# Performance work log

Hardware: AMD Instinct MI355X
Metric: run time of the kernel (lower is better)

Reference implementation:

```python
import jax, jax.numpy as jnp
import numpy as np

N_NODES = 100000
D = 128        # hidden_channels
H = 64         # hidden_size
E = 8192       # num_hyperedges
K = 32         # nodes per hyperedge (fixed group size)


def setup_inputs() -> dict:
    key = jax.random.key(0)
    k1, k2, k3, k4, k5, k6 = jax.random.split(key, 6)
    X = jax.random.normal(k1, (N_NODES, D), dtype=jnp.float32)
    idx = jax.random.randint(k2, (E, K), 0, N_NODES, dtype=jnp.int64)
    # per-hyperedge MLP params (torch Linear: y = x @ W.T + b), scaled like
    # torch's default uniform fan-in init magnitude
    W1 = jax.random.normal(k3, (E, H, D), dtype=jnp.float32) / np.sqrt(D)
    b1 = jax.random.normal(k4, (E, H), dtype=jnp.float32) / np.sqrt(D)
    W2 = jax.random.normal(k5, (E, H), dtype=jnp.float32) / np.sqrt(H)
    b2 = jax.random.normal(k6, (E,), dtype=jnp.float32) / np.sqrt(H)
    return {"X": X, "idx": idx, "W1": W1, "b1": b1, "W2": W2, "b2": b2}


def reference(X, idx, W1, b1, W2, b2):
    # gather node features per hyperedge: [E, K, D]
    x_he = X[idx]
    # per-edge 2-layer MLP scorer (leaky_relu slope 0.01 = torch default)
    h = jax.nn.leaky_relu(jnp.einsum('ekd,ehd->ekh', x_he, W1) + b1[:, None, :])
    w = jnp.einsum('ekh,eh->ek', h, W2) + b2[:, None]          # [E, K]
    beta = jax.nn.softmax(w, axis=1)                           # softmax over group
    z = jnp.einsum('ek,ekd->ed', beta, x_he)                   # weighted sum reduce
    Z = jnp.tanh(jax.nn.leaky_relu(z))                         # [E, D]
    return Z, beta
```

## Files before the change

kernel.cpp:

```cpp
#include <hip/hip_runtime.h>

#define E_EDGES 8192
#define KN 32
#define DD 128
#define HH 64
#define XPAD 8
#define EPB 4
#define NBLK (E_EDGES / EPB)

typedef __attribute__((ext_vector_type(8))) __bf16 bf16x8;
typedef __attribute__((ext_vector_type(4))) __bf16 bf16x4;
typedef __attribute__((ext_vector_type(4))) float f32x4;

__device__ __forceinline__ void sync_lds() {
    asm volatile("s_waitcnt lgkmcnt(0)" ::: "memory");
    __builtin_amdgcn_s_barrier();
    __builtin_amdgcn_sched_barrier(0);
}

__global__ __launch_bounds__(256, 4)
void he_attn_kernel(const float* __restrict__ X,
                    const int* __restrict__ idx,
                    const float* __restrict__ W1,
                    const float* __restrict__ b1,
                    const float* __restrict__ W2,
                    const float* __restrict__ b2,
                    float* __restrict__ Zout,
                    float* __restrict__ Bout)
{
    const int tid  = threadIdx.x;
    const int lane = tid & 63;
    const int wv   = tid >> 6;
    const int cl   = lane & 15;
    const int kg   = lane >> 4;
    const int ebase = blockIdx.x * EPB;

    const int r0 = tid >> 5;
    const int c0 = (tid & 31) * 4;
    const int j  = wv * 16 + cl;

    __shared__ unsigned short xsb[KN][DD + XPAD];
    __shared__ float wpart[4][KN];
    __shared__ float beta_s[KN];

    float b1v[EPB], w2v[EPB], b2v[EPB];
    #pragma unroll
    for (int t = 0; t < EPB; ++t) {
        b1v[t] = b1[(size_t)(ebase + t) * HH + j];
        w2v[t] = W2[(size_t)(ebase + t) * HH + j];
        b2v[t] = b2[ebase + t];
    }
    int rowc[4];
    #pragma unroll
    for (int it = 0; it < 4; ++it) rowc[it] = idx[(size_t)ebase * KN + r0 + 8 * it];
    float4 xr[4];
    #pragma unroll
    for (int it = 0; it < 4; ++it)
        xr[it] = *reinterpret_cast<const float4*>(X + (size_t)rowc[it] * DD + c0);
    float4 wf[8];
    {
        const float* W1r = W1 + ((size_t)ebase * HH + j) * DD;
        #pragma unroll
        for (int q = 0; q < 8; ++q)
            wf[q] = *reinterpret_cast<const float4*>(W1r + (q >> 1) * 32 + kg * 8 + (q & 1) * 4);
    }
    int rown[4];
    #pragma unroll
    for (int it = 0; it < 4; ++it)
        rown[it] = idx[(size_t)(ebase + 1) * KN + r0 + 8 * it];

    #pragma unroll
    for (int t = 0; t < EPB; ++t) {
        const int e = ebase + t;

        bf16x8 bb[4];
        #pragma unroll
        for (int kc = 0; kc < 4; ++kc) {
            float4 a = wf[2 * kc], b = wf[2 * kc + 1];
            bf16x8 v;
            v[0] = (__bf16)a.x; v[1] = (__bf16)a.y; v[2] = (__bf16)a.z; v[3] = (__bf16)a.w;
            v[4] = (__bf16)b.x; v[5] = (__bf16)b.y; v[6] = (__bf16)b.z; v[7] = (__bf16)b.w;
            bb[kc] = v;
        }

        sync_lds();

        #pragma unroll
        for (int it = 0; it < 4; ++it) {
            bf16x4 bv;
            bv[0] = (__bf16)xr[it].x; bv[1] = (__bf16)xr[it].y;
            bv[2] = (__bf16)xr[it].z; bv[3] = (__bf16)xr[it].w;
            *reinterpret_cast<bf16x4*>(&xsb[r0 + 8 * it][c0]) = bv;
        }

        if (t + 1 < EPB) {
            #pragma unroll
            for (int it = 0; it < 4; ++it)
                xr[it] = *reinterpret_cast<const float4*>(X + (size_t)rown[it] * DD + c0);
            const float* W1r = W1 + ((size_t)(e + 1) * HH + j) * DD;
            #pragma unroll
            for (int q = 0; q < 8; ++q)
                wf[q] = *reinterpret_cast<const float4*>(W1r + (q >> 1) * 32 + kg * 8 + (q & 1) * 4);
        }
        if (t + 2 < EPB) {
            #pragma unroll
            for (int it = 0; it < 4; ++it)
                rown[it] = idx[(size_t)(e + 2) * KN + r0 + 8 * it];
        }

        sync_lds();

        f32x4 acc0 = {0.f, 0.f, 0.f, 0.f}, acc1 = {0.f, 0.f, 0.f, 0.f};
        #pragma unroll
        for (int kc = 0; kc < 4; ++kc) {
            const int ds = kc * 32 + kg * 8;
            bf16x8 a0 = *reinterpret_cast<const bf16x8*>(&xsb[cl][ds]);
            bf16x8 a1 = *reinterpret_cast<const bf16x8*>(&xsb[16 + cl][ds]);
            acc0 = __builtin_amdgcn_mfma_f32_16x16x32_bf16(a0, bb[kc], acc0, 0, 0, 0);
            acc1 = __builtin_amdgcn_mfma_f32_16x16x32_bf16(a1, bb[kc], acc1, 0, 0, 0);
        }

        float pk[8];
        #pragma unroll
        for (int r = 0; r < 4; ++r) {
            float h0 = acc0[r] + b1v[t]; h0 = (h0 > 0.f) ? h0 : 0.01f * h0;
            float h1 = acc1[r] + b1v[t]; h1 = (h1 > 0.f) ? h1 : 0.01f * h1;
            pk[r]     = h0 * w2v[t];
            pk[4 + r] = h1 * w2v[t];
        }
        #pragma unroll
        for (int m = 1; m < 16; m <<= 1) {
            #pragma unroll
            for (int q = 0; q < 8; ++q) pk[q] += __shfl_xor(pk[q], m);
        }
        if (cl == 0) {
            #pragma unroll
            for (int r = 0; r < 4; ++r) {
                wpart[wv][kg * 4 + r]      = pk[r];
                wpart[wv][16 + kg * 4 + r] = pk[4 + r];
            }
        }

        sync_lds();

        if (tid < KN) {
            float v = b2v[t] + wpart[0][tid] + wpart[1][tid] + wpart[2][tid] + wpart[3][tid];
            float mx = v;
            #pragma unroll
            for (int off = 16; off >= 1; off >>= 1) mx = fmaxf(mx, __shfl_xor(mx, off));
            float ex = __expf(v - mx);
            float s = ex;
            #pragma unroll
            for (int off = 16; off >= 1; off >>= 1) s += __shfl_xor(s, off);
            float beta = ex / s;
            beta_s[tid] = beta;
            Bout[(size_t)e * KN + tid] = beta;
        }

        sync_lds();

        if (tid < DD) {
            float z = 0.f;
            #pragma unroll
            for (int k = 0; k < KN; ++k) {
                unsigned int bq = xsb[k][tid];
                z += beta_s[k] * __builtin_bit_cast(float, bq << 16);
            }
            z = (z > 0.f) ? z : 0.01f * z;
            Zout[(size_t)e * DD + tid] = tanhf(z);
        }
    }
}

extern "C" void kernel_launch(void* const* d_in, const int* in_sizes, int n_in,
                              void* d_out, int out_size, void* d_ws, size_t ws_size,
                              hipStream_t stream) {
    const float* X   = (const float*)d_in[0];
    const int*   idx = (const int*)d_in[1];
    const float* W1  = (const float*)d_in[2];
    const float* b1  = (const float*)d_in[3];
    const float* W2  = (const float*)d_in[4];
    const float* b2  = (const float*)d_in[5];
    float* Zout = (float*)d_out;
    float* Bout = Zout + (size_t)E_EDGES * DD;
    (void)in_sizes; (void)n_in; (void)out_size; (void)d_ws; (void)ws_size;
    he_attn_kernel<<<dim3(NBLK), dim3(256), 0, stream>>>(X, idx, W1, b1, W2, b2, Zout, Bout);
}
```

Baseline: 67.14 us.

## Assign one hyperedge per wavefront and replace block barriers with wave sync

Each wavefront now processes a whole hyperedge independently, doing its own gather, all four 16-wide H tiles of the MFMA scorer, softmax and weighted sum. This replaces the old layout where the four waves of a block split the H dimension of one edge and stepped through four edges in sequence. Block-wide barriers become wave-level syncs and the cross-wave partial-score reduction disappears. The cost is four times the LDS per block, less software prefetch across edges, and more serial MFMA work per wave.

```diff
diff --git a/kernel.cpp b/kernel.cpp
--- a/kernel.cpp
+++ b/kernel.cpp
@@ -4,18 +4,19 @@
 #define KN 32
 #define DD 128
 #define HH 64
-#define XPAD 8
-#define EPB 4
-#define NBLK (E_EDGES / EPB)
+#define XSTR (DD + 8)
 
 typedef __attribute__((ext_vector_type(8))) __bf16 bf16x8;
 typedef __attribute__((ext_vector_type(4))) __bf16 bf16x4;
 typedef __attribute__((ext_vector_type(4))) float f32x4;
 
-__device__ __forceinline__ void sync_lds() {
+__device__ __forceinline__ float bf2f(unsigned int u) {
+    return __builtin_bit_cast(float, u << 16);
+}
+
+__device__ __forceinline__ void wave_sync_lds() {
     asm volatile("s_waitcnt lgkmcnt(0)" ::: "memory");
-    __builtin_amdgcn_s_barrier();
-    __builtin_amdgcn_sched_barrier(0);
+    __builtin_amdgcn_wave_barrier();
 }
 
 __global__ __launch_bounds__(256, 4)
@@ -31,48 +32,59 @@
     const int tid  = threadIdx.x;
     const int lane = tid & 63;
     const int wv   = tid >> 6;
+    const int e    = blockIdx.x * 4 + wv;
     const int cl   = lane & 15;
     const int kg   = lane >> 4;
-    const int ebase = blockIdx.x * EPB;
 
-    const int r0 = tid >> 5;
-    const int c0 = (tid & 31) * 4;
-    const int j  = wv * 16 + cl;
+    __shared__ __align__(16) unsigned short xsb[4][KN][XSTR];
+    __shared__ __align__(16) float ws[4][KN];
 
-    __shared__ unsigned short xsb[KN][DD + XPAD];
-    __shared__ float wpart[4][KN];
-    __shared__ float beta_s[KN];
+    const int iv = idx[(size_t)e * KN + (lane & 31)];
+    float b1v[4], w2v[4];
+    #pragma unroll
+    for (int jt = 0; jt < 4; ++jt) {
+        b1v[jt] = b1[(size_t)e * HH + jt * 16 + cl];
+        w2v[jt] = W2[(size_t)e * HH + jt * 16 + cl];
+    }
+    const float b2v = b2[e];
 
-    float b1v[EPB], w2v[EPB], b2v[EPB];
+    const float* W1e = W1 + (size_t)e * HH * DD;
+    float4 wf[8];
     #pragma unroll
-    for (int t = 0; t < EPB; ++t) {
-        b1v[t] = b1[(size_t)(ebase + t) * HH + j];
-        w2v[t] = W2[(size_t)(ebase + t) * HH + j];
-        b2v[t] = b2[ebase + t];
+    for (int q = 0; q < 8; ++q)
+        wf[q] = *reinterpret_cast<const float4*>(
+            W1e + (size_t)cl * DD + (q >> 1) * 32 + kg * 8 + (q & 1) * 4);
+
+    const int rb = lane >> 5;
+    const int cc = lane & 31;
+    #pragma unroll
+    for (int hb = 0; hb < 2; ++hb) {
+        float4 xr[8];
+        #pragma unroll
+        for (int q = 0; q < 8; ++q) {
+            int row = __shfl(iv, rb + 2 * (hb * 8 + q));
+            xr[q] = reinterpret_cast<const float4*>(X)[(size_t)row * (DD / 4) + cc];
+        }
+        #pragma unroll
+        for (int q = 0; q < 8; ++q) {
+            bf16x4 bv;
+            bv[0] = (__bf16)xr[q].x; bv[1] = (__bf16)xr[q].y;
+            bv[2] = (__bf16)xr[q].z; bv[3] = (__bf16)xr[q].w;
+            *reinterpret_cast<bf16x4*>(&xsb[wv][rb + 2 * (hb * 8 + q)][cc * 4]) = bv;
+        }
     }
-    int rowc[4];
+    wave_sync_lds();
+
+    bf16x8 a0[4], a1[4];
     #pragma unroll
-    for (int it = 0; it < 4; ++it) rowc[it] = idx[(size_t)ebase * KN + r0 + 8 * it];
-    float4 xr[4];
+    for (int kc = 0; kc < 4; ++kc) {
+        a0[kc] = *reinterpret_cast<const bf16x8*>(&xsb[wv][cl][kc * 32 + kg * 8]);
+        a1[kc] = *reinterpret_cast<const bf16x8*>(&xsb[wv][16 + cl][kc * 32 + kg * 8]);
+    }
+
+    float pk[8] = {0.f,0.f,0.f,0.f,0.f,0.f,0.f,0.f};
     #pragma unroll
-    for (int it = 0; it < 4; ++it)
-        xr[it] = *reinterpret_cast<const float4*>(X + (size_t)rowc[it] * DD + c0);
-    float4 wf[8];
-    {
-        const float* W1r = W1 + ((size_t)ebase * HH + j) * DD;
-        #pragma unroll
-        for (int q = 0; q < 8; ++q)
-            wf[q] = *reinterpret_cast<const float4*>(W1r + (q >> 1) * 32 + kg * 8 + (q & 1) * 4);
-    }
-    int rown[4];
-    #pragma unroll
-    for (int it = 0; it < 4; ++it)
-        rown[it] = idx[(size_t)(ebase + 1) * KN + r0 + 8 * it];
-
-    #pragma unroll
-    for (int t = 0; t < EPB; ++t) {
-        const int e = ebase + t;
-
+    for (int jt = 0; jt < 4; ++jt) {
         bf16x8 bb[4];
         #pragma unroll
         for (int kc = 0; kc < 4; ++kc) {
@@ -82,94 +94,77 @@
             v[4] = (__bf16)b.x; v[5] = (__bf16)b.y; v[6] = (__bf16)b.z; v[7] = (__bf16)b.w;
             bb[kc] = v;
         }
-
-        sync_lds();
-
-        #pragma unroll
-        for (int it = 0; it < 4; ++it) {
-            bf16x4 bv;
-            bv[0] = (__bf16)xr[it].x; bv[1] = (__bf16)xr[it].y;
-            bv[2] = (__bf16)xr[it].z; bv[3] = (__bf16)xr[it].w;
-            *reinterpret_cast<bf16x4*>(&xsb[r0 + 8 * it][c0]) = bv;
-        }
-
-        if (t + 1 < EPB) {
-            #pragma unroll
-            for (int it = 0; it < 4; ++it)
-                xr[it] = *reinterpret_cast<const float4*>(X + (size_t)rown[it] * DD + c0);
-            const float* W1r = W1 + ((size_t)(e + 1) * HH + j) * DD;
+        if (jt < 3) {
+            const float* W1r = W1e + (size_t)((jt + 1) * 16 + cl) * DD;
             #pragma unroll
             for (int q = 0; q < 8; ++q)
-                wf[q] = *reinterpret_cast<const float4*>(W1r + (q >> 1) * 32 + kg * 8 + (q & 1) * 4);
+                wf[q] = *reinterpret_cast<const float4*>(
+                    W1r + (q >> 1) * 32 + kg * 8 + (q & 1) * 4);
         }
-        if (t + 2 < EPB) {
-            #pragma unroll
-            for (int it = 0; it < 4; ++it)
-                rown[it] = idx[(size_t)(e + 2) * KN + r0 + 8 * it];
-        }
-
-        sync_lds();
-
-        f32x4 acc0 = {0.f, 0.f, 0.f, 0.f}, acc1 = {0.f, 0.f, 0.f, 0.f};
+        f32x4 acc0 = {0.f,0.f,0.f,0.f}, acc1 = {0.f,0.f,0.f,0.f};
         #pragma unroll
         for (int kc = 0; kc < 4; ++kc) {
-            const int ds = kc * 32 + kg * 8;
-            bf16x8 a0 = *reinterpret_cast<const bf16x8*>(&xsb[cl][ds]);
-            bf16x8 a1 = *reinterpret_cast<const bf16x8*>(&xsb[16 + cl][ds]);
-            acc0 = __builtin_amdgcn_mfma_f32_16x16x32_bf16(a0, bb[kc], acc0, 0, 0, 0);
-            acc1 = __builtin_amdgcn_mfma_f32_16x16x32_bf16(a1, bb[kc], acc1, 0, 0, 0);
+            acc0 = __builtin_amdgcn_mfma_f32_16x16x32_bf16(a0[kc], bb[kc], acc0, 0, 0, 0);
+            acc1 = __builtin_amdgcn_mfma_f32_16x16x32_bf16(a1[kc], bb[kc], acc1, 0, 0, 0);
         }
-
-        float pk[8];
         #pragma unroll
         for (int r = 0; r < 4; ++r) {
-            float h0 = acc0[r] + b1v[t]; h0 = (h0 > 0.f) ? h0 : 0.01f * h0;
-            float h1 = acc1[r] + b1v[t]; h1 = (h1 > 0.f) ? h1 : 0.01f * h1;
-            pk[r]     = h0 * w2v[t];
-            pk[4 + r] = h1 * w2v[t];
-        }
-        #pragma unroll
-        for (int m = 1; m < 16; m <<= 1) {
-            #pragma unroll
-            for (int q = 0; q < 8; ++q) pk[q] += __shfl_xor(pk[q], m);
-        }
-        if (cl == 0) {
-            #pragma unroll
-            for (int r = 0; r < 4; ++r) {
-                wpart[wv][kg * 4 + r]      = pk[r];
-                wpart[wv][16 + kg * 4 + r] = pk[4 + r];
-            }
-        }
-
-        sync_lds();
-
-        if (tid < KN) {
-            float v = b2v[t] + wpart[0][tid] + wpart[1][tid] + wpart[2][tid] + wpart[3][tid];
-            float mx = v;
-            #pragma unroll
-            for (int off = 16; off >= 1; off >>= 1) mx = fmaxf(mx, __shfl_xor(mx, off));
-            float ex = __expf(v - mx);
-            float s = ex;
-            #pragma unroll
-            for (int off = 16; off >= 1; off >>= 1) s += __shfl_xor(s, off);
-            float beta = ex / s;
-            beta_s[tid] = beta;
-            Bout[(size_t)e * KN + tid] = beta;
-        }
-
-        sync_lds();
-
-        if (tid < DD) {
-            float z = 0.f;
-            #pragma unroll
-            for (int k = 0; k < KN; ++k) {
-                unsigned int bq = xsb[k][tid];
-                z += beta_s[k] * __builtin_bit_cast(float, bq << 16);
-            }
-            z = (z > 0.f) ? z : 0.01f * z;
-            Zout[(size_t)e * DD + tid] = tanhf(z);
+            float h0 = acc0[r] + b1v[jt]; h0 = (h0 > 0.f) ? h0 : 0.01f * h0;
+            float h1 = acc1[r] + b1v[jt]; h1 = (h1 > 0.f) ? h1 : 0.01f * h1;
+            pk[r]     += h0 * w2v[jt];
+            pk[4 + r] += h1 * w2v[jt];
         }
     }
+    #pragma unroll
+    for (int m = 1; m < 16; m <<= 1) {
+        #pragma unroll
+        for (int q = 0; q < 8; ++q) pk[q] += __shfl_xor(pk[q], m);
+    }
+    if (cl == 0) {
+        #pragma unroll
+        for (int r = 0; r < 4; ++r) {
+            ws[wv][kg * 4 + r]      = pk[r];
+            ws[wv][16 + kg * 4 + r] = pk[4 + r];
+        }
+    }
+    wave_sync_lds();
+
+    {
+        const int k = lane & 31;
+        float v = ws[wv][k] + b2v;
+        float mx = v;
+        #pragma unroll
+        for (int off = 16; off >= 1; off >>= 1) mx = fmaxf(mx, __shfl_xor(mx, off));
+        float ex = __expf(v - mx);
+        float s = ex;
+        #pragma unroll
+        for (int off = 16; off >= 1; off >>= 1) s += __shfl_xor(s, off);
+        float beta = ex / s;
+        if (lane < 32) {
+            ws[wv][k] = beta;
+            Bout[(size_t)e * KN + k] = beta;
+        }
+    }
+    wave_sync_lds();
+
+    float z0 = 0.f, z1 = 0.f;
+    #pragma unroll
+    for (int kq = 0; kq < 8; ++kq) {
+        f32x4 bq = *reinterpret_cast<const f32x4*>(&ws[wv][kq * 4]);
+        #pragma unroll
+        for (int r = 0; r < 4; ++r) {
+            unsigned int pr = *reinterpret_cast<const unsigned int*>(
+                &xsb[wv][kq * 4 + r][2 * lane]);
+            z0 += bq[r] * bf2f(pr & 0xffffu);
+            z1 += bq[r] * bf2f(pr >> 16);
+        }
+    }
+    z0 = (z0 > 0.f) ? z0 : 0.01f * z0;
+    z1 = (z1 > 0.f) ? z1 : 0.01f * z1;
+    float2 outv;
+    outv.x = tanhf(z0);
+    outv.y = tanhf(z1);
+    *reinterpret_cast<float2*>(&Zout[(size_t)e * DD + 2 * lane]) = outv;
 }
 
 extern "C" void kernel_launch(void* const* d_in, const int* in_sizes, int n_in,
@@ -184,5 +179,5 @@
     float* Zout = (float*)d_out;
     float* Bout = Zout + (size_t)E_EDGES * DD;
     (void)in_sizes; (void)n_in; (void)out_size; (void)d_ws; (void)ws_size;
-    he_attn_kernel<<<dim3(NBLK), dim3(256), 0, stream>>>(X, idx, W1, b1, W2, b2, Zout, Bout);
+    he_attn_kernel<<<dim3(E_EDGES / 4), dim3(256), 0, stream>>>(X, idx, W1, b1, W2, b2, Zout, Bout);
 }
```

Result: no change. 66.45 us (-1.0%).
